# Kernel optimization log

Hardware: AMD Instinct MI355X
Metric: run time of the kernel (lower is better)

The kernel has to match this reference:

```python
import jax, jax.numpy as jnp
import numpy as np

HIDDEN = 2304
N_HEADS = 8
N_KV_HEADS = 4
HEAD_DIM = 256
SLIDING_WINDOW = 4096
QUERY_PRE_ATTN_SCALAR = 256.0
SOFTCAP = 50.0
ROPE_BASE = 10000.0


def setup_inputs() -> dict:
    key = jax.random.key(0)
    ks = jax.random.split(key, 6)
    B, S = 1, 4096
    scale = 0.02
    return {
        "hidden_states": jax.random.normal(ks[0], (B, S, HIDDEN), dtype=jnp.float32),
        "Wq": jax.random.normal(ks[1], (HIDDEN, N_HEADS * HEAD_DIM), dtype=jnp.float32) * scale,
        "Wk": jax.random.normal(ks[2], (HIDDEN, N_KV_HEADS * HEAD_DIM), dtype=jnp.float32) * scale,
        "Wv": jax.random.normal(ks[3], (HIDDEN, N_KV_HEADS * HEAD_DIM), dtype=jnp.float32) * scale,
        "Wo": jax.random.normal(ks[4], (N_HEADS * HEAD_DIM, HIDDEN), dtype=jnp.float32) * scale,
        "position_ids": jnp.arange(S, dtype=jnp.int64 if jax.config.jax_enable_x64 else jnp.int32)[None, :],
    }


def _rope_cos_sin(position_ids):
    # inv_freq: (head_dim//2,)
    inv_freq = 1.0 / (ROPE_BASE ** (jnp.arange(0, HEAD_DIM, 2, dtype=jnp.float32) / HEAD_DIM))
    freqs = position_ids.astype(jnp.float32)[..., None] * inv_freq[None, None, :]  # (B,S,hd/2)
    emb = jnp.concatenate([freqs, freqs], axis=-1)  # (B,S,hd)
    return jnp.cos(emb), jnp.sin(emb)


def _rotate_half(x):
    x1, x2 = jnp.split(x, 2, axis=-1)
    return jnp.concatenate([-x2, x1], axis=-1)


def reference(hidden_states, Wq, Wk, Wv, Wo, position_ids):
    B, S, _ = hidden_states.shape
    cos, sin = _rope_cos_sin(position_ids)  # (B,S,hd)
    cos = cos[:, None]  # (B,1,S,hd) broadcast over heads
    sin = sin[:, None]

    q = (hidden_states @ Wq).reshape(B, S, N_HEADS, HEAD_DIM).transpose(0, 2, 1, 3)
    k = (hidden_states @ Wk).reshape(B, S, N_KV_HEADS, HEAD_DIM).transpose(0, 2, 1, 3)
    v = (hidden_states @ Wv).reshape(B, S, N_KV_HEADS, HEAD_DIM).transpose(0, 2, 1, 3)

    q = q * cos + _rotate_half(q) * sin
    k = k * cos + _rotate_half(k) * sin

    # GQA: repeat kv heads to match query heads
    n_rep = N_HEADS // N_KV_HEADS
    k = jnp.repeat(k, n_rep, axis=1)  # (B,H,S,hd)
    v = jnp.repeat(v, n_rep, axis=1)

    scaling = QUERY_PRE_ATTN_SCALAR ** -0.5
    scores = jnp.einsum("bhqd,bhkd->bhqk", q, k) * scaling

    # attention logit softcapping
    scores = SOFTCAP * jnp.tanh(scores / SOFTCAP)

    # causal + sliding window mask
    qi = jnp.arange(S)[:, None]
    kj = jnp.arange(S)[None, :]
    mask = (kj <= qi) & (qi - kj < SLIDING_WINDOW)  # (S,S)
    scores = jnp.where(mask[None, None], scores, jnp.asarray(-1e30, scores.dtype))

    attn = jax.nn.softmax(scores, axis=-1)
    ctx = jnp.einsum("bhqk,bhkd->bhqd", attn, v)  # (B,H,S,hd)
    ctx = ctx.transpose(0, 2, 1, 3).reshape(B, S, N_HEADS * HEAD_DIM)
    return ctx @ Wo
```

## Files before the change

kernel.cpp:

```cpp
#include <hip/hip_runtime.h>
#include <cstdint>
#include <cstddef>

typedef unsigned short u16;
typedef short bf16x8 __attribute__((ext_vector_type(8)));
typedef float f32x4 __attribute__((ext_vector_type(4)));

#define S_LEN 4096
#define HID   2304
#define NH    8
#define NKV   4
#define HD    256
#define QD    2048
#define KD    1024
#define QKVW  4096
#define CHT   32
#define SLOTS_PER_HEAD 160

__device__ __forceinline__ u16 f2b(float f) {
    union { float f; uint32_t u; } v; v.f = f;
    uint32_t r = (v.u + 0x7FFFu + ((v.u >> 16) & 1u)) >> 16;
    return (u16)r;
}
__device__ __forceinline__ float b2f(u16 u) {
    union { uint32_t u; float f; } v; v.u = ((uint32_t)u) << 16;
    return v.f;
}

__device__ __forceinline__ void glds16(const void* g, void* l) {
    __builtin_amdgcn_global_load_lds(
        (__attribute__((address_space(1))) void*)(const_cast<void*>(g)),
        (__attribute__((address_space(3))) void*)l, 16, 0, 0);
}

__device__ __forceinline__ int slot_base(int qt) {
    int a = qt >> 4, b = qt & 15;
    return (a + 1) * (8 * a + b);
}

__device__ __forceinline__ float softcap_p(float s) {
    float u = s * 0.00125f;
    u = fminf(fmaxf(u, -0.53f), 0.53f);
    float u2 = u * u;
    float t50 = u * (50.0f + u2 * (-16.6666667f + 6.66666667f * u2));
    return __expf(t50);
}

__device__ __forceinline__ void twcvt_body(const float* __restrict__ W, u16* __restrict__ out,
                                           int K, int N, int ldo, int n0, int k0, float (*T)[68]) {
    const int t = threadIdx.x;
    for (int i = 0; i < 4; i++) {
        int id = i * 256 + t;
        int r = id >> 4, c4 = id & 15;
        float4 v = *(const float4*)(W + (size_t)(k0 + r) * N + n0 + c4 * 4);
        *(float4*)(&T[r][c4 * 4]) = v;
    }
    __syncthreads();
    for (int i = 0; i < 4; i++) {
        int id = i * 256 + t;
        int rn = id >> 4, c4 = id & 15;
        u16 a = f2b(T[c4 * 4 + 0][rn]);
        u16 b = f2b(T[c4 * 4 + 1][rn]);
        u16 c = f2b(T[c4 * 4 + 2][rn]);
        u16 d = f2b(T[c4 * 4 + 3][rn]);
        uint2 o;
        o.x = (uint32_t)a | ((uint32_t)b << 16);
        o.y = (uint32_t)c | ((uint32_t)d << 16);
        *(uint2*)(out + (size_t)(n0 + rn) * ldo + k0 + c4 * 4) = o;
    }
}

#define PREP_CVT   9216
#define PREP_QKV   3456
#define PREP_WO    1152
__global__ __launch_bounds__(256) void prep_all(const float* __restrict__ H,
                                                const float* __restrict__ Wq,
                                                const float* __restrict__ Wk,
                                                const float* __restrict__ Wv,
                                                const float* __restrict__ Wo,
                                                u16* __restrict__ Hb,
                                                u16* __restrict__ Wqkvt,
                                                u16* __restrict__ Wot) {
    __shared__ float T[64][68];
    const int bid = blockIdx.x;
    if (bid < PREP_CVT) {
        int id = bid * 256 + threadIdx.x;
        float4 v = ((const float4*)H)[id];
        uint2 o;
        o.x = (uint32_t)f2b(v.x) | ((uint32_t)f2b(v.y) << 16);
        o.y = (uint32_t)f2b(v.z) | ((uint32_t)f2b(v.w) << 16);
        ((uint2*)Hb)[id] = o;
    } else if (bid < PREP_CVT + PREP_QKV) {
        int b = bid - PREP_CVT;
        int bx = b & 31; int rest = b >> 5; int by = rest % 36; int z = rest / 36;
        const float* W = (z == 0) ? Wq : (z == 1) ? Wk : Wv;
        const int N = (z == 0) ? QD : KD;
        const int n0 = bx * 64;
        if (n0 >= N) return;
        u16* ob = Wqkvt + ((z == 0) ? 0 : (z == 1) ? (size_t)QD * HID : (size_t)(QD + KD) * HID);
        twcvt_body(W, ob, HID, N, HID, n0, by * 64, T);
    } else {
        int b = bid - PREP_CVT - PREP_QKV;
        int bx = b % 36, by = b / 36;
        twcvt_body(Wo, Wot, QD, HID, QD, bx * 64, by * 64, T);
    }
}

template<int BF16_OUT>
__global__ __launch_bounds__(512, 2) void gemm256(const u16* __restrict__ A, const u16* __restrict__ B,
                                                  void* __restrict__ Cp, int M, int N, int K) {
    const int tid = threadIdx.x;
    const int wv = tid >> 6, lane = tid & 63;
    const int quad = lane >> 4, m16 = lane & 15;
    const int gx = gridDim.x;
    int bid = blockIdx.y * gx + blockIdx.x;
    const int cpx = (gx * gridDim.y) >> 3;
    bid = (bid & 7) * cpx + (bid >> 3);
    const int m0 = (bid / gx) * 256, n0 = (bid % gx) * 256;
    const int wm = (wv & 1) * 128, wn = (wv >> 1) * 64;

    __shared__ __align__(16) u16 As[2][256 * 64];
    __shared__ __align__(16) u16 Bs[2][256 * 64];

    const int lr = lane >> 3, ls = lane & 7;
    const int scol = ((ls ^ lr) << 3);
    const u16* pA[4]; const u16* pB[4];
    int du[4];
#pragma unroll
    for (int j = 0; j < 4; j++) {
        int u = wv + 8 * j;
        pA[j] = A + (size_t)(m0 + u * 8 + lr) * K + scol;
        pB[j] = B + (size_t)(n0 + u * 8 + lr) * K + scol;
        du[j] = u * 512;
    }

    f32x4 acc[8][4];
#pragma unroll
    for (int i = 0; i < 8; i++)
#pragma unroll
        for (int j = 0; j < 4; j++) acc[i][j] = (f32x4){0.f, 0.f, 0.f, 0.f};

    const int aBase = (wm + m16) * 64;
    const int bBase = (wn + m16) * 64;
    const int s0 = ((quad ^ (m16 & 7)) << 3);
    const int s1 = s0 ^ 32;

    const int NT = K >> 6;
#pragma unroll
    for (int j = 0; j < 4; j++) glds16(pA[j], &As[0][du[j]]);
#pragma unroll
    for (int j = 0; j < 4; j++) glds16(pB[j], &Bs[0][du[j]]);
    asm volatile("s_waitcnt vmcnt(0)" ::: "memory");
    __builtin_amdgcn_sched_barrier(0);
    __builtin_amdgcn_s_barrier();

    for (int t = 0; t < NT; t++) {
        const int cur = t & 1, nxt = cur ^ 1;
        const int kn = (t + 1) << 6;
        const bool pre = (t + 1 < NT);
        bf16x8 af[4], bf[4];

#define MFMA16(IOFF)                                                               \
        _Pragma("unroll")                                                          \
        for (int i = 0; i < 4; i++)                                                \
            _Pragma("unroll")                                                      \
            for (int j = 0; j < 4; j++)                                            \
                acc[i + (IOFF)][j] =                                               \
                    __builtin_amdgcn_mfma_f32_16x16x32_bf16(af[i], bf[j],          \
                                                            acc[i + (IOFF)][j], 0, 0, 0);
#define PHASE_SYNC()                                                               \
        __builtin_amdgcn_s_barrier();                                              \
        asm volatile("s_waitcnt lgkmcnt(0)" ::: "memory");                         \
        __builtin_amdgcn_sched_barrier(0);

#pragma unroll
        for (int i = 0; i < 4; i++) af[i] = *(const bf16x8*)(&As[cur][aBase + i * 1024 + s0]);
#pragma unroll
        for (int j = 0; j < 4; j++) bf[j] = *(const bf16x8*)(&Bs[cur][bBase + j * 1024 + s0]);
        if (pre) {
#pragma unroll
            for (int j = 0; j < 4; j++) glds16(pA[j] + kn, &As[nxt][du[j]]);
        }
        PHASE_SYNC();
        __builtin_amdgcn_s_setprio(1);
        MFMA16(0);
        __builtin_amdgcn_s_setprio(0);
        __builtin_amdgcn_s_barrier();
#pragma unroll
        for (int i = 0; i < 4; i++) af[i] = *(const bf16x8*)(&As[cur][aBase + (i + 4) * 1024 + s0]);
        if (pre) {
#pragma unroll
            for (int j = 0; j < 4; j++) glds16(pB[j] + kn, &Bs[nxt][du[j]]);
        }
        PHASE_SYNC();
        __builtin_amdgcn_s_setprio(1);
        MFMA16(4);
        __builtin_amdgcn_s_setprio(0);
        __builtin_amdgcn_s_barrier();
#pragma unroll
        for (int i = 0; i < 4; i++) af[i] = *(const bf16x8*)(&As[cur][aBase + i * 1024 + s1]);
#pragma unroll
        for (int j = 0; j < 4; j++) bf[j] = *(const bf16x8*)(&Bs[cur][bBase + j * 1024 + s1]);
        PHASE_SYNC();
        __builtin_amdgcn_s_setprio(1);
        MFMA16(0);
        __builtin_amdgcn_s_setprio(0);
        __builtin_amdgcn_s_barrier();
#pragma unroll
        for (int i = 0; i < 4; i++) af[i] = *(const bf16x8*)(&As[cur][aBase + (i + 4) * 1024 + s1]);
        PHASE_SYNC();
        __builtin_amdgcn_s_setprio(1);
        MFMA16(4);
        __builtin_amdgcn_s_setprio(0);
        asm volatile("s_waitcnt vmcnt(0)" ::: "memory");
        __builtin_amdgcn_sched_barrier(0);
        __builtin_amdgcn_s_barrier();
#undef MFMA16
#undef PHASE_SYNC
    }
#pragma unroll
    for (int i = 0; i < 8; i++)
#pragma unroll
        for (int j = 0; j < 4; j++)
#pragma unroll
            for (int r = 0; r < 4; r++) {
                int row = m0 + wm + i * 16 + quad * 4 + r;
                int col = n0 + wn + j * 16 + m16;
                if (BF16_OUT) ((u16*)Cp)[(size_t)row * N + col] = f2b(acc[i][j][r]);
                else          ((float*)Cp)[(size_t)row * N + col] = acc[i][j][r];
            }
}

template<int BF16_OUT>
__global__ __launch_bounds__(256, 2) void gemm_bt(const u16* __restrict__ A, const u16* __restrict__ B,
                                                  void* __restrict__ Cp, int M, int N, int K) {
    const int tid  = threadIdx.x;
    const int wv = tid >> 6, lane = tid & 63;
    const int quad = lane >> 4, m16 = lane & 15;
    const int gx = gridDim.x;
    int bid = blockIdx.y * gx + blockIdx.x;
    const int cpx = (gx * gridDim.y) >> 3;
    bid = (bid & 7) * cpx + (bid >> 3);
    const int m0 = (bid / gx) * 128, n0 = (bid % gx) * 128;
    const int wm = (wv & 1) * 64, wn = (wv >> 1) * 64;
    __shared__ __align__(16) u16 As[128 * 32];
    __shared__ __align__(16) u16 Bs[128 * 32];
    int s0i = (wv * 2) * 64 + lane, s1i = s0i + 64;
    int row0 = s0i >> 2, c0 = (s0i & 3) ^ (row0 & 3);
    int row1 = s1i >> 2, c1 = (s1i & 3) ^ (row1 & 3);
    const u16* pA0 = A + (size_t)(m0 + row0) * K + c0 * 8;
    const u16* pA1 = A + (size_t)(m0 + row1) * K + c1 * 8;
    const u16* pB0 = B + (size_t)(n0 + row0) * K + c0 * 8;
    const u16* pB1 = B + (size_t)(n0 + row1) * K + c1 * 8;
    u16* lA0 = &As[(wv * 2 + 0) * 512]; u16* lA1 = &As[(wv * 2 + 1) * 512];
    u16* lB0 = &Bs[(wv * 2 + 0) * 512]; u16* lB1 = &Bs[(wv * 2 + 1) * 512];

    const f32x4 z4 = {0.f, 0.f, 0.f, 0.f};
    f32x4 acc00 = z4, acc01 = z4, acc02 = z4, acc03 = z4;
    f32x4 acc10 = z4, acc11 = z4, acc12 = z4, acc13 = z4;
    f32x4 acc20 = z4, acc21 = z4, acc22 = z4, acc23 = z4;
    f32x4 acc30 = z4, acc31 = z4, acc32 = z4, acc33 = z4;

    const int sw = quad ^ (m16 & 3);
    const u16* ra0 = &As[(wm + 0 * 16 + m16) * 32 + (sw << 3)];
    const u16* ra1 = &As[(wm + 1 * 16 + m16) * 32 + (sw << 3)];
    const u16* ra2 = &As[(wm + 2 * 16 + m16) * 32 + (sw << 3)];
    const u16* ra3 = &As[(wm + 3 * 16 + m16) * 32 + (sw << 3)];
    const u16* rb0 = &Bs[(wn + 0 * 16 + m16) * 32 + (sw << 3)];
    const u16* rb1 = &Bs[(wn + 1 * 16 + m16) * 32 + (sw << 3)];
    const u16* rb2 = &Bs[(wn + 2 * 16 + m16) * 32 + (sw << 3)];
    const u16* rb3 = &Bs[(wn + 3 * 16 + m16) * 32 + (sw << 3)];

    for (int k0 = 0; k0 < K; k0 += 32) {
        __syncthreads();
        glds16(pA0 + k0, lA0);
        glds16(pA1 + k0, lA1);
        glds16(pB0 + k0, lB0);
        glds16(pB1 + k0, lB1);
        __syncthreads();
        bf16x8 af0 = *(const bf16x8*)ra0, af1 = *(const bf16x8*)ra1;
        bf16x8 af2 = *(const bf16x8*)ra2, af3 = *(const bf16x8*)ra3;
        bf16x8 bf0 = *(const bf16x8*)rb0, bf1 = *(const bf16x8*)rb1;
        bf16x8 bf2 = *(const bf16x8*)rb2, bf3 = *(const bf16x8*)rb3;
        acc00 = __builtin_amdgcn_mfma_f32_16x16x32_bf16(af0, bf0, acc00, 0, 0, 0);
        acc01 = __builtin_amdgcn_mfma_f32_16x16x32_bf16(af0, bf1, acc01, 0, 0, 0);
        acc02 = __builtin_amdgcn_mfma_f32_16x16x32_bf16(af0, bf2, acc02, 0, 0, 0);
        acc03 = __builtin_amdgcn_mfma_f32_16x16x32_bf16(af0, bf3, acc03, 0, 0, 0);
        acc10 = __builtin_amdgcn_mfma_f32_16x16x32_bf16(af1, bf0, acc10, 0, 0, 0);
        acc11 = __builtin_amdgcn_mfma_f32_16x16x32_bf16(af1, bf1, acc11, 0, 0, 0);
        acc12 = __builtin_amdgcn_mfma_f32_16x16x32_bf16(af1, bf2, acc12, 0, 0, 0);
        acc13 = __builtin_amdgcn_mfma_f32_16x16x32_bf16(af1, bf3, acc13, 0, 0, 0);
        acc20 = __builtin_amdgcn_mfma_f32_16x16x32_bf16(af2, bf0, acc20, 0, 0, 0);
        acc21 = __builtin_amdgcn_mfma_f32_16x16x32_bf16(af2, bf1, acc21, 0, 0, 0);
        acc22 = __builtin_amdgcn_mfma_f32_16x16x32_bf16(af2, bf2, acc22, 0, 0, 0);
        acc23 = __builtin_amdgcn_mfma_f32_16x16x32_bf16(af2, bf3, acc23, 0, 0, 0);
        acc30 = __builtin_amdgcn_mfma_f32_16x16x32_bf16(af3, bf0, acc30, 0, 0, 0);
        acc31 = __builtin_amdgcn_mfma_f32_16x16x32_bf16(af3, bf1, acc31, 0, 0, 0);
        acc32 = __builtin_amdgcn_mfma_f32_16x16x32_bf16(af3, bf2, acc32, 0, 0, 0);
        acc33 = __builtin_amdgcn_mfma_f32_16x16x32_bf16(af3, bf3, acc33, 0, 0, 0);
    }

#define STORE_TILE(I, J, ACC)                                              \
    {                                                                      \
        _Pragma("unroll")                                                  \
        for (int r = 0; r < 4; r++) {                                      \
            int row = m0 + wm + (I) * 16 + quad * 4 + r;                   \
            int col = n0 + wn + (J) * 16 + m16;                            \
            float v = (ACC)[r];                                            \
            if (BF16_OUT) ((u16*)Cp)[(size_t)row * N + col] = f2b(v);      \
            else          ((float*)Cp)[(size_t)row * N + col] = v;         \
        }                                                                  \
    }
    STORE_TILE(0, 0, acc00) STORE_TILE(0, 1, acc01) STORE_TILE(0, 2, acc02) STORE_TILE(0, 3, acc03)
    STORE_TILE(1, 0, acc10) STORE_TILE(1, 1, acc11) STORE_TILE(1, 2, acc12) STORE_TILE(1, 3, acc13)
    STORE_TILE(2, 0, acc20) STORE_TILE(2, 1, acc21) STORE_TILE(2, 2, acc22) STORE_TILE(2, 3, acc23)
    STORE_TILE(3, 0, acc30) STORE_TILE(3, 1, acc31) STORE_TILE(3, 2, acc32) STORE_TILE(3, 3, acc33)
#undef STORE_TILE
}

#define RV_ROPE 2048
__global__ __launch_bounds__(256) void rope_vtrans(const u16* __restrict__ QKV, const int* __restrict__ pos,
                                                   u16* __restrict__ Qb, u16* __restrict__ Kb,
                                                   u16* __restrict__ Vt) {
    const int bid = blockIdx.x;
    if (bid < RV_ROPE) {
        int id = bid * 256 + threadIdx.x;
        int s = id >> 7, j = id & 127;
        float p = (float)pos[s];
        float invf = expf(-0.07195578429985445f * (float)j);
        float ang = p * invf;
        float sn, cs;
        sincosf(ang, &sn, &cs);
        const u16* src = QKV + (size_t)s * QKVW;
        u16* dq = Qb + (size_t)s * QD;
#pragma unroll
        for (int h = 0; h < NH; h++) {
            float x1 = b2f(src[h * 256 + j]), x2 = b2f(src[h * 256 + 128 + j]);
            dq[h * 256 + j]       = f2b(x1 * cs - x2 * sn);
            dq[h * 256 + 128 + j] = f2b(x2 * cs + x1 * sn);
        }
        const u16* sk = src + QD;
        u16* dk = Kb + (size_t)s * KD;
#pragma unroll
        for (int h = 0; h < NKV; h++) {
            float x1 = b2f(sk[h * 256 + j]), x2 = b2f(sk[h * 256 + 128 + j]);
            dk[h * 256 + j]       = f2b(x1 * cs - x2 * sn);
            dk[h * 256 + 128 + j] = f2b(x2 * cs + x1 * sn);
        }
    } else {
        __shared__ u16 T[64][72];
        int vb = bid - RV_ROPE;
        const int s0 = (vb & 63) * 64, d0 = (vb >> 6) * 64;
        const int t = threadIdx.x;
        for (int i = 0; i < 2; i++) {
            int id = i * 256 + t;
            int r = id >> 3, c = id & 7;
            uint4 v = *(const uint4*)(QKV + (size_t)(s0 + r) * QKVW + (QD + KD) + d0 + c * 8);
            *(uint4*)(&T[r][c * 8]) = v;
        }
        __syncthreads();
        for (int i = 0; i < 2; i++) {
            int id = i * 256 + t;
            int r = id >> 3, c = id & 7;
            union { u16 u[8]; uint4 v; } o;
            for (int jj = 0; jj < 8; jj++) o.u[jj] = T[c * 8 + jj][r];
            *(uint4*)(Vt + (size_t)(d0 + r) * S_LEN + s0 + c * 8) = o.v;
        }
    }
}

__global__ __launch_bounds__(256, 3) void attn_part(const u16* __restrict__ Qb, const u16* __restrict__ Kb,
                                                    const u16* __restrict__ Vt,
                                                    u16* __restrict__ Part, float* __restrict__ Lpart) {
    const int tid  = threadIdx.x;
    const int wv = tid >> 6, lane = tid & 63;
    const int quad = lane >> 4, m16 = lane & 15;
    const int bid = blockIdx.x;
    const int xc = bid >> 3;
    const int h  = bid & 7;
    const int qt = 63 - (xc >> 2);
    const int ch = xc & 3;
    const int n_kvt = 2 * qt + 2;
    const int t0 = ch * CHT;
    if (t0 >= n_kvt) return;
    const int t1 = min(t0 + CHT, n_kvt);
    const int kvh = h >> 1;
    const int q0 = qt * 64;
    const int slot = h * SLOTS_PER_HEAD + slot_base(qt) + ch;

    __shared__ __align__(16) u16 Kl[2][32 * 256];
    __shared__ __align__(16) u16 Vl[256 * 32];
    __shared__ __align__(16) u16 Pl[4][16 * 32];

    int kOff[4], vOff[4];
#pragma unroll
    for (int i = 0; i < 4; i++) {
        int s = (wv * 4 + i) * 64 + lane;
        int kv = s >> 5, c = (s & 31) ^ (kv & 7);
        kOff[i] = kv * KD + c * 8;
        int d = s >> 2, cc = (s & 3) ^ ((d >> 1) & 3);
        vOff[i] = d * S_LEN + cc * 8;
    }
    const u16* Kbase = Kb + kvh * 256;
    const u16* Vbase = Vt + (size_t)(kvh * 256) * S_LEN;

    bf16x8 qf[8];
    {
        const u16* qp = Qb + (size_t)(q0 + wv * 16 + m16) * QD + h * 256 + quad * 8;
#pragma unroll
        for (int ks = 0; ks < 8; ks++) qf[ks] = *(const bf16x8*)(qp + ks * 32);
    }
    float li[4] = {0.f, 0.f, 0.f, 0.f};
    f32x4 o[4][4];
#pragma unroll
    for (int i = 0; i < 4; i++)
#pragma unroll
        for (int j = 0; j < 4; j++) o[i][j] = (f32x4){0.f, 0.f, 0.f, 0.f};

#pragma unroll
    for (int i = 0; i < 4; i++)
        glds16(Kbase + kOff[i] + t0 * (32 * KD), &Kl[0][(wv * 4 + i) * 512]);

    for (int kt = t0; kt < t1; kt++) {
        const int cur = (kt - t0) & 1, nxt = cur ^ 1;
        asm volatile("s_waitcnt vmcnt(0)" ::: "memory");
        __builtin_amdgcn_sched_barrier(0);
        __builtin_amdgcn_s_barrier();
#pragma unroll
        for (int i = 0; i < 4; i++)
            glds16(Vbase + vOff[i] + kt * 32, &Vl[(wv * 4 + i) * 512]);
        if (kt + 1 < t1) {
#pragma unroll
            for (int i = 0; i < 4; i++)
                glds16(Kbase + kOff[i] + (kt + 1) * (32 * KD), &Kl[nxt][(wv * 4 + i) * 512]);
        }
        f32x4 s[2];
        __builtin_amdgcn_s_setprio(1);
#pragma unroll
        for (int nt = 0; nt < 2; nt++) {
            f32x4 a = (f32x4){0.f, 0.f, 0.f, 0.f};
            int kr = nt * 16 + m16;
            int sw = kr & 7;
#pragma unroll
            for (int ks = 0; ks < 8; ks++) {
                int c = ks * 4 + quad;
                bf16x8 kf = *(const bf16x8*)(&Kl[cur][kr * 256 + ((c ^ sw) << 3)]);
                a = __builtin_amdgcn_mfma_f32_16x16x32_bf16(qf[ks], kf, a, 0, 0, 0);
            }
            s[nt] = a;
        }
        __builtin_amdgcn_s_setprio(0);
        const int kvb = kt * 32;
        u16* Pw = &Pl[wv][0];
        if (kvb + 31 <= q0) {
#pragma unroll
            for (int nt = 0; nt < 2; nt++)
#pragma unroll
                for (int r = 0; r < 4; r++) {
                    float p = softcap_p(s[nt][r]);
                    li[r] += p;
                    int m = quad * 4 + r;
                    int c = 2 * nt + (m16 >> 3);
                    int off = m16 & 7;
                    Pw[m * 32 + ((c ^ ((m >> 1) & 3)) << 3) + off] = f2b(p);
                }
        } else {
#pragma unroll
            for (int nt = 0; nt < 2; nt++)
#pragma unroll
                for (int r = 0; r < 4; r++) {
                    float p = softcap_p(s[nt][r]);
                    int kvg = kvb + nt * 16 + m16;
                    int qg  = q0 + wv * 16 + quad * 4 + r;
                    p = (kvg > qg) ? 0.f : p;
                    li[r] += p;
                    int m = quad * 4 + r;
                    int c = 2 * nt + (m16 >> 3);
                    int off = m16 & 7;
                    Pw[m * 32 + ((c ^ ((m >> 1) & 3)) << 3) + off] = f2b(p);
                }
        }
        if (kt + 1 < t1) {
            asm volatile("s_waitcnt vmcnt(4) lgkmcnt(0)" ::: "memory");
        } else {
            asm volatile("s_waitcnt vmcnt(0) lgkmcnt(0)" ::: "memory");
        }
        __builtin_amdgcn_sched_barrier(0);
        __builtin_amdgcn_s_barrier();
        bf16x8 pf[4];
#pragma unroll
        for (int qs = 0; qs < 4; qs++)
            pf[qs] = *(const bf16x8*)(&Pl[qs][m16 * 32 + ((quad ^ ((m16 >> 1) & 3)) << 3)]);
        __builtin_amdgcn_s_setprio(1);
#pragma unroll
        for (int dt = 0; dt < 4; dt++) {
            int d = wv * 64 + dt * 16 + m16;
            bf16x8 vf = *(const bf16x8*)(&Vl[d * 32 + ((quad ^ ((d >> 1) & 3)) << 3)]);
            o[0][dt] = __builtin_amdgcn_mfma_f32_16x16x32_bf16(pf[0], vf, o[0][dt], 0, 0, 0);
            o[1][dt] = __builtin_amdgcn_mfma_f32_16x16x32_bf16(pf[1], vf, o[1][dt], 0, 0, 0);
            o[2][dt] = __builtin_amdgcn_mfma_f32_16x16x32_bf16(pf[2], vf, o[2][dt], 0, 0, 0);
            o[3][dt] = __builtin_amdgcn_mfma_f32_16x16x32_bf16(pf[3], vf, o[3][dt], 0, 0, 0);
        }
        __builtin_amdgcn_s_setprio(0);
    }
    u16* Pp = Part + (size_t)slot * (64 * 256);
#pragma unroll
    for (int qs = 0; qs < 4; qs++)
#pragma unroll
        for (int dt = 0; dt < 4; dt++)
#pragma unroll
            for (int r = 0; r < 4; r++)
                Pp[(qs * 16 + quad * 4 + r) * 256 + wv * 64 + dt * 16 + m16] = f2b(o[qs][dt][r]);
#pragma unroll
    for (int r = 0; r < 4; r++) {
        float l = li[r];
        l += __shfl_xor(l, 1); l += __shfl_xor(l, 2);
        l += __shfl_xor(l, 4); l += __shfl_xor(l, 8);
        if (m16 == 0) Lpart[slot * 64 + wv * 16 + quad * 4 + r] = l;
    }
}

__global__ __launch_bounds__(256) void attn_combine(const u16* __restrict__ Part,
                                                    const float* __restrict__ Lpart,
                                                    u16* __restrict__ Ctx) {
    const int qt = 63 - blockIdx.x;
    const int h = blockIdx.y;
    const int nch = (qt >> 4) + 1;
    const int slot0 = h * SLOTS_PER_HEAD + slot_base(qt);
    const int t = threadIdx.x;
    const int q0 = qt * 64;
    __shared__ float linv[64];
    if (t < 64) {
        float l = 0.f;
        for (int c = 0; c < nch; c++) l += Lpart[(slot0 + c) * 64 + t];
        linv[t] = 1.f / l;
    }
    __syncthreads();
    const u16* P0 = Part + (size_t)slot0 * (64 * 256);
    for (int i = 0; i < 8; i++) {
        int idx = i * 256 + t;
        int row = idx >> 5, c8 = idx & 31;
        float acc[8] = {0.f,0.f,0.f,0.f,0.f,0.f,0.f,0.f};
        for (int c = 0; c < nch; c++) {
            uint4 v = *(const uint4*)(P0 + (size_t)c * (64 * 256) + row * 256 + c8 * 8);
            uint32_t w[4] = {v.x, v.y, v.z, v.w};
            for (int k = 0; k < 4; k++) {
                acc[k * 2]     += b2f((u16)(w[k] & 0xFFFF));
                acc[k * 2 + 1] += b2f((u16)(w[k] >> 16));
            }
        }
        float iv = linv[row];
        uint4 ov;
        uint32_t* op = (uint32_t*)&ov;
        for (int k = 0; k < 4; k++)
            op[k] = (uint32_t)f2b(acc[k * 2] * iv) | ((uint32_t)f2b(acc[k * 2 + 1] * iv) << 16);
        *(uint4*)(Ctx + (size_t)(q0 + row) * QD + h * 256 + c8 * 8) = ov;
    }
}

extern "C" void kernel_launch(void* const* d_in, const int* in_sizes, int n_in,
                              void* d_out, int out_size, void* d_ws, size_t ws_size,
                              hipStream_t stream) {
    const float* H  = (const float*)d_in[0];
    const float* Wq = (const float*)d_in[1];
    const float* Wk = (const float*)d_in[2];
    const float* Wv = (const float*)d_in[3];
    const float* Wo = (const float*)d_in[4];
    const int* pos  = (const int*)d_in[5];
    float* out = (float*)d_out;

    char* ws = (char*)d_ws;
    size_t off = 0;
    u16* Hb     = (u16*)(ws + off); off += (size_t)S_LEN * HID * 2;
    u16* Wqkvt  = (u16*)(ws + off); off += (size_t)QKVW * HID * 2;
    u16* Wot    = (u16*)(ws + off); off += (size_t)HID * QD * 2;
    u16* QKVraw = (u16*)(ws + off); off += (size_t)S_LEN * QKVW * 2;
    u16* Qb     = (u16*)(ws + off); off += (size_t)S_LEN * QD * 2;
    u16* Kb     = (u16*)(ws + off); off += (size_t)S_LEN * KD * 2;
    u16* Vt     = (u16*)(ws + off); off += (size_t)KD * S_LEN * 2;
    u16* Ctx    = (u16*)(ws + off); off += (size_t)S_LEN * QD * 2;
    u16* Part   = (u16*)(ws + off);  off += (size_t)NH * SLOTS_PER_HEAD * 64 * 256 * 2;
    float* Lprt = (float*)(ws + off); off += (size_t)NH * SLOTS_PER_HEAD * 64 * 4;

    prep_all<<<dim3(PREP_CVT + PREP_QKV + PREP_WO), dim3(256), 0, stream>>>(H, Wq, Wk, Wv, Wo, Hb, Wqkvt, Wot);
    gemm256<1><<<dim3(QKVW / 256, S_LEN / 256), dim3(512), 0, stream>>>(Hb, Wqkvt, QKVraw, S_LEN, QKVW, HID);
    rope_vtrans<<<dim3(RV_ROPE + 1024), dim3(256), 0, stream>>>(QKVraw, pos, Qb, Kb, Vt);
    attn_part<<<dim3(2048), dim3(256), 0, stream>>>(Qb, Kb, Vt, Part, Lprt);
    attn_combine<<<dim3(64, NH), dim3(256), 0, stream>>>(Part, Lprt, Ctx);
    gemm_bt<0><<<dim3(HID / 128, S_LEN / 128), dim3(256), 0, stream>>>(Ctx, Wot, out, S_LEN, HID, QD);
}
```

Baseline: 459.6 us.

## Load V fragments directly to registers and drop heaviest-first block ordering

The attention kernel no longer stages V tiles through LDS. Each wave now reads its V MFMA operands straight from global memory into registers at the top of every KV step, which removes the V LDS buffer, its offset math and the vmcnt wait before the PV product. The launch also switches from a flattened, heaviest-query-tile-first ordering to a plain 3D grid (qt, head, chunk), so light tiles are scheduled first. This risks worse tail load balance, and the register-held V loads add VGPR pressure and more uncoalesced global traffic.

```diff
diff --git a/kernel.cpp b/kernel.cpp
--- a/kernel.cpp
+++ b/kernel.cpp
@@ -375,11 +375,7 @@
     const int tid  = threadIdx.x;
     const int wv = tid >> 6, lane = tid & 63;
     const int quad = lane >> 4, m16 = lane & 15;
-    const int bid = blockIdx.x;
-    const int xc = bid >> 3;
-    const int h  = bid & 7;
-    const int qt = 63 - (xc >> 2);
-    const int ch = xc & 3;
+    const int qt = blockIdx.x, h = blockIdx.y, ch = blockIdx.z;
     const int n_kvt = 2 * qt + 2;
     const int t0 = ch * CHT;
     if (t0 >= n_kvt) return;
@@ -389,20 +385,17 @@
     const int slot = h * SLOTS_PER_HEAD + slot_base(qt) + ch;
 
     __shared__ __align__(16) u16 Kl[2][32 * 256];
-    __shared__ __align__(16) u16 Vl[256 * 32];
     __shared__ __align__(16) u16 Pl[4][16 * 32];
 
-    int kOff[4], vOff[4];
+    int kOff[4];
 #pragma unroll
     for (int i = 0; i < 4; i++) {
         int s = (wv * 4 + i) * 64 + lane;
         int kv = s >> 5, c = (s & 31) ^ (kv & 7);
         kOff[i] = kv * KD + c * 8;
-        int d = s >> 2, cc = (s & 3) ^ ((d >> 1) & 3);
-        vOff[i] = d * S_LEN + cc * 8;
     }
     const u16* Kbase = Kb + kvh * 256;
-    const u16* Vbase = Vt + (size_t)(kvh * 256) * S_LEN;
+    const u16* Vfb = Vt + (size_t)(kvh * 256 + wv * 64 + m16) * S_LEN + quad * 8;
 
     bf16x8 qf[8];
     {
@@ -426,9 +419,11 @@
         asm volatile("s_waitcnt vmcnt(0)" ::: "memory");
         __builtin_amdgcn_sched_barrier(0);
         __builtin_amdgcn_s_barrier();
-#pragma unroll
-        for (int i = 0; i < 4; i++)
-            glds16(Vbase + vOff[i] + kt * 32, &Vl[(wv * 4 + i) * 512]);
+        bf16x8 vfr[4];
+#pragma unroll
+        for (int dt = 0; dt < 4; dt++)
+            vfr[dt] = *(const bf16x8*)(Vfb + (size_t)dt * (16 * S_LEN) + kt * 32);
+        __builtin_amdgcn_sched_barrier(0);
         if (kt + 1 < t1) {
 #pragma unroll
             for (int i = 0; i < 4; i++)
@@ -480,11 +475,7 @@
                     Pw[m * 32 + ((c ^ ((m >> 1) & 3)) << 3) + off] = f2b(p);
                 }
         }
-        if (kt + 1 < t1) {
-            asm volatile("s_waitcnt vmcnt(4) lgkmcnt(0)" ::: "memory");
-        } else {
-            asm volatile("s_waitcnt vmcnt(0) lgkmcnt(0)" ::: "memory");
-        }
+        asm volatile("s_waitcnt lgkmcnt(0)" ::: "memory");
         __builtin_amdgcn_sched_barrier(0);
         __builtin_amdgcn_s_barrier();
         bf16x8 pf[4];
@@ -494,12 +485,10 @@
         __builtin_amdgcn_s_setprio(1);
 #pragma unroll
         for (int dt = 0; dt < 4; dt++) {
-            int d = wv * 64 + dt * 16 + m16;
-            bf16x8 vf = *(const bf16x8*)(&Vl[d * 32 + ((quad ^ ((d >> 1) & 3)) << 3)]);
-            o[0][dt] = __builtin_amdgcn_mfma_f32_16x16x32_bf16(pf[0], vf, o[0][dt], 0, 0, 0);
-            o[1][dt] = __builtin_amdgcn_mfma_f32_16x16x32_bf16(pf[1], vf, o[1][dt], 0, 0, 0);
-            o[2][dt] = __builtin_amdgcn_mfma_f32_16x16x32_bf16(pf[2], vf, o[2][dt], 0, 0, 0);
-            o[3][dt] = __builtin_amdgcn_mfma_f32_16x16x32_bf16(pf[3], vf, o[3][dt], 0, 0, 0);
+            o[0][dt] = __builtin_amdgcn_mfma_f32_16x16x32_bf16(pf[0], vfr[dt], o[0][dt], 0, 0, 0);
+            o[1][dt] = __builtin_amdgcn_mfma_f32_16x16x32_bf16(pf[1], vfr[dt], o[1][dt], 0, 0, 0);
+            o[2][dt] = __builtin_amdgcn_mfma_f32_16x16x32_bf16(pf[2], vfr[dt], o[2][dt], 0, 0, 0);
+            o[3][dt] = __builtin_amdgcn_mfma_f32_16x16x32_bf16(pf[3], vfr[dt], o[3][dt], 0, 0, 0);
         }
         __builtin_amdgcn_s_setprio(0);
     }
@@ -523,8 +512,7 @@
 __global__ __launch_bounds__(256) void attn_combine(const u16* __restrict__ Part,
                                                     const float* __restrict__ Lpart,
                                                     u16* __restrict__ Ctx) {
-    const int qt = 63 - blockIdx.x;
-    const int h = blockIdx.y;
+    const int qt = blockIdx.x, h = blockIdx.y;
     const int nch = (qt >> 4) + 1;
     const int slot0 = h * SLOTS_PER_HEAD + slot_base(qt);
     const int t = threadIdx.x;
@@ -585,7 +573,7 @@
     prep_all<<<dim3(PREP_CVT + PREP_QKV + PREP_WO), dim3(256), 0, stream>>>(H, Wq, Wk, Wv, Wo, Hb, Wqkvt, Wot);
     gemm256<1><<<dim3(QKVW / 256, S_LEN / 256), dim3(512), 0, stream>>>(Hb, Wqkvt, QKVraw, S_LEN, QKVW, HID);
     rope_vtrans<<<dim3(RV_ROPE + 1024), dim3(256), 0, stream>>>(QKVraw, pos, Qb, Kb, Vt);
-    attn_part<<<dim3(2048), dim3(256), 0, stream>>>(Qb, Kb, Vt, Part, Lprt);
+    attn_part<<<dim3(64, NH, 4), dim3(256), 0, stream>>>(Qb, Kb, Vt, Part, Lprt);
     attn_combine<<<dim3(64, NH), dim3(256), 0, stream>>>(Part, Lprt, Ctx);
     gemm_bt<0><<<dim3(HID / 128, S_LEN / 128), dim3(256), 0, stream>>>(Ctx, Wot, out, S_LEN, HID, QD);
 }
```

Result: faster. 439.6 us (-4.4%).
